# Kernel optimization log

Measured on AMD Instinct MI355X. Metric: run time of the kernel, lower is better.

The kernel has to match this reference:

```python
import jax, jax.numpy as jnp
import numpy as np

DIM = 1536
HEADS = 12
HEAD_DIM = 128
SEQ = 3120
FRAME = 1560
EPS = 1e-6


def _rmsnorm(x, gamma, eps=EPS):
    var = jnp.mean(jnp.square(x), axis=-1, keepdims=True)
    return x * jax.lax.rsqrt(var + eps) * gamma


def _rope(x, cos, sin):
    # x: [B,S,H,D], cos/sin: [S, D//2]; rotate interleaved pairs (Wan-style)
    xr = x.reshape(x.shape[:-1] + (x.shape[-1] // 2, 2))
    x1, x2 = xr[..., 0], xr[..., 1]
    c = cos[None, :, None, :]
    s = sin[None, :, None, :]
    o1 = x1 * c - x2 * s
    o2 = x1 * s + x2 * c
    return jnp.stack([o1, o2], axis=-1).reshape(x.shape)


def setup_inputs() -> dict:
    key = jax.random.key(0)
    ks = jax.random.split(key, 8)
    pos = jnp.arange(SEQ, dtype=jnp.float32)[:, None]
    inv_freq = 1.0 / (10000.0 ** (jnp.arange(0, HEAD_DIM // 2, dtype=jnp.float32) / (HEAD_DIM // 2)))
    ang = pos * inv_freq[None, :]
    return {
        "hidden_states": jax.random.normal(ks[0], (1, SEQ, DIM), jnp.float32),
        "freqs_cos": jnp.cos(ang),
        "freqs_sin": jnp.sin(ang),
        "w_qkv": jax.random.normal(ks[1], (DIM, 3 * DIM), jnp.float32) * (DIM ** -0.5),
        "b_qkv": jnp.zeros((3 * DIM,), jnp.float32),
        "g_q": jnp.ones((DIM,), jnp.float32),
        "g_k": jnp.ones((DIM,), jnp.float32),
        "w_out": jax.random.normal(ks[2], (DIM, DIM), jnp.float32) * (DIM ** -0.5),
        "b_out": jnp.zeros((DIM,), jnp.float32),
        "frame_len": FRAME,
    }


def reference(hidden_states, freqs_cos, freqs_sin, w_qkv, b_qkv, g_q, g_k, w_out, b_out, frame_len):
    B, S, _ = hidden_states.shape
    qkv = hidden_states @ w_qkv + b_qkv  # [B,S,3*DIM]
    q, k, v = jnp.split(qkv, 3, axis=-1)
    q = _rmsnorm(q, g_q)
    k = _rmsnorm(k, g_k)
    q = q.reshape(B, S, HEADS, HEAD_DIM)
    k = k.reshape(B, S, HEADS, HEAD_DIM)
    v = v.reshape(B, S, HEADS, HEAD_DIM)
    q = _rope(q, freqs_cos, freqs_sin)
    k = _rope(k, freqs_cos, freqs_sin)
    # block-wise causal mask over frames of frame_len tokens
    blk = jnp.arange(S) // frame_len
    mask = blk[None, :] <= blk[:, None]  # [Sq, Sk]
    scale = 1.0 / jnp.sqrt(jnp.float32(HEAD_DIM))
    scores = jnp.einsum("bqhd,bkhd->bhqk", q, k) * scale
    scores = jnp.where(mask[None, None], scores, jnp.float32(-1e30))
    probs = jax.nn.softmax(scores, axis=-1)
    out = jnp.einsum("bhqk,bkhd->bqhd", probs, v)
    out = out.reshape(B, S, HEADS * HEAD_DIM)
    return out @ w_out + b_out
```

## Files before the change

### kernel.cpp

```cpp
#include <hip/hip_runtime.h>
#include <hip/hip_bf16.h>
#include <stdint.h>

#define SEQ_LEN 3120
#define DIM 1536
#define QKV_N 4608
#define HEADS 12
#define HEAD_DIM 128
#define FRAME_LEN 1560
#define SM_SCALE 0.08838834764831845f
#define LOG2E 1.4426950408889634f
#define FMAXC2 43.280851226669165f
#define BQ 256

#if __has_builtin(__builtin_amdgcn_exp2f)
#define FEXP2(x) __builtin_amdgcn_exp2f(x)
#else
#define FEXP2(x) exp2f(x)
#endif

typedef short short8 __attribute__((ext_vector_type(8)));
typedef float f32x4 __attribute__((ext_vector_type(4)));
typedef float f32x16 __attribute__((ext_vector_type(16)));

__device__ __forceinline__ unsigned short f2bf(float x) {
    union { float f; unsigned u; } v; v.f = x;
    unsigned r = v.u + 0x7fffu + ((v.u >> 16) & 1u);
    return (unsigned short)(r >> 16);
}
__device__ __forceinline__ float bf2f(unsigned short b) {
    union { unsigned u; float f; } v; v.u = ((unsigned)b) << 16;
    return v.f;
}
__device__ __forceinline__ unsigned pk2bf(float a, float b) {
    __hip_bfloat162 h = __float22bfloat162_rn(make_float2(a, b));
    union { __hip_bfloat162 h2; unsigned u; } v; v.h2 = h;
    return v.u;
}

__device__ __forceinline__ void async16(void* lds, const void* g) {
    __builtin_amdgcn_global_load_lds(
        (const __attribute__((address_space(1))) unsigned int*)g,
        (__attribute__((address_space(3))) unsigned int*)lds, 16, 0, 0);
}

__device__ __forceinline__ void transpose_tile(
    const float* __restrict__ in, unsigned short* __restrict__ out,
    int R, int C, int c0, int r0, float (*T)[65], int tid)
{
    const int rl = tid >> 4, cl = (tid & 15) * 4;
#pragma unroll
    for (int i = 0; i < 4; ++i) {
        const int row = r0 + rl + i * 16;
        float4 v = *(const float4*)&in[(size_t)row * C + c0 + cl];
        T[cl + 0][rl + i * 16] = v.x; T[cl + 1][rl + i * 16] = v.y;
        T[cl + 2][rl + i * 16] = v.z; T[cl + 3][rl + i * 16] = v.w;
    }
    __syncthreads();
    const int oc = tid >> 2, ob = (tid & 3) * 16;
    union { unsigned short t[16]; uint4 u[2]; } p;
#pragma unroll
    for (int j = 0; j < 16; ++j) p.t[j] = f2bf(T[oc][ob + j]);
    uint4* dst = (uint4*)&out[(size_t)(c0 + oc) * R + r0 + ob];
    dst[0] = p.u[0];
    dst[1] = p.u[1];
}

__global__ __launch_bounds__(256) void prep_kernel(
    const float* __restrict__ hs, unsigned short* __restrict__ hsb,
    const float* __restrict__ w_qkv, unsigned short* __restrict__ wqkvT,
    const float* __restrict__ w_out, unsigned short* __restrict__ woutT)
{
    __shared__ float T[64][65];
    const int bid = blockIdx.x;
    const int tid = threadIdx.x;
    if (bid < 2340) {
        const int i = bid * 256 + tid;
        const float4 a = ((const float4*)hs)[i * 2];
        const float4 b = ((const float4*)hs)[i * 2 + 1];
        union { unsigned short t[8]; uint4 u; } p;
        p.t[0] = f2bf(a.x); p.t[1] = f2bf(a.y); p.t[2] = f2bf(a.z); p.t[3] = f2bf(a.w);
        p.t[4] = f2bf(b.x); p.t[5] = f2bf(b.y); p.t[6] = f2bf(b.z); p.t[7] = f2bf(b.w);
        ((uint4*)hsb)[i] = p.u;
    } else if (bid < 4068) {
        const int t = bid - 2340;
        transpose_tile(w_qkv, wqkvT, DIM, QKV_N, (t % 72) * 64, (t / 72) * 64, T, tid);
    } else {
        const int t = bid - 4068;
        transpose_tile(w_out, woutT, DIM, DIM, (t % 24) * 64, (t / 24) * 64, T, tid);
    }
}

__global__ __launch_bounds__(256, 2) void gemm_bt_kernel(
    const unsigned short* __restrict__ A, const unsigned short* __restrict__ Bt,
    const float* __restrict__ bias, float* __restrict__ C, int M, int N, int K,
    int ntp, int spx)
{
    __shared__ short As[2][4096];
    __shared__ short Bs[2][4096];

    const int xcd = blockIdx.x & 7;
    const int idx = (xcd & 1) * spx + (blockIdx.x >> 3);
    const int mtiles = (M + 127) >> 7;
    if (idx >= ntp * mtiles) return;
    const int m0 = (idx / ntp) * 128;
    const int n0 = ((xcd >> 1) * ntp + idx % ntp) * 128;

    const int tid = threadIdx.x;
    const int w = tid >> 6, l = tid & 63;
    const int wr = w >> 1, wc = w & 1;
    const int lhi = l >> 4, llo = l & 15;

    f32x4 acc[4][4];
#pragma unroll
    for (int i = 0; i < 4; ++i)
#pragma unroll
        for (int j = 0; j < 4; ++j) acc[i][j] = f32x4{0.f, 0.f, 0.f, 0.f};

    const int c0i = (w * 2) * 64 + l, c1i = c0i + 64;
    const unsigned short* gA0 = A + (size_t)min(m0 + (c0i >> 2), M - 1) * K + (c0i & 3) * 8;
    const unsigned short* gA1 = A + (size_t)min(m0 + (c1i >> 2), M - 1) * K + (c1i & 3) * 8;
    const unsigned short* gB0 = Bt + (size_t)(n0 + (c0i >> 2)) * K + (c0i & 3) * 8;
    const unsigned short* gB1 = Bt + (size_t)(n0 + (c1i >> 2)) * K + (c1i & 3) * 8;

    const int aoff = (wr * 64 + llo) * 32 + lhi * 8;
    const int boff = (wc * 64 + llo) * 32 + lhi * 8;

    auto stage = [&](int k0, int b) {
        async16(As[b] + (w * 2 + 0) * 512, gA0 + k0);
        async16(As[b] + (w * 2 + 1) * 512, gA1 + k0);
        async16(Bs[b] + (w * 2 + 0) * 512, gB0 + k0);
        async16(Bs[b] + (w * 2 + 1) * 512, gB1 + k0);
    };

    const int nk = K >> 5;
    stage(0, 0);
    for (int t = 0; t < nk; ++t) {
        __syncthreads();
        if (t + 1 < nk) stage((t + 1) * 32, (t + 1) & 1);
        const short* A_ = As[t & 1];
        const short* B_ = Bs[t & 1];
        short8 af[4], bf[4];
#pragma unroll
        for (int mt = 0; mt < 4; ++mt) af[mt] = *(const short8*)&A_[aoff + mt * 512];
#pragma unroll
        for (int nt = 0; nt < 4; ++nt) bf[nt] = *(const short8*)&B_[boff + nt * 512];
#pragma unroll
        for (int mt = 0; mt < 4; ++mt)
#pragma unroll
            for (int nt = 0; nt < 4; ++nt)
                acc[mt][nt] = __builtin_amdgcn_mfma_f32_16x16x32_bf16(af[mt], bf[nt], acc[mt][nt], 0, 0, 0);
    }

#pragma unroll
    for (int mt = 0; mt < 4; ++mt)
#pragma unroll
        for (int ri = 0; ri < 4; ++ri) {
            const int row = m0 + wr * 64 + mt * 16 + lhi * 4 + ri;
            if (row < M) {
#pragma unroll
                for (int nt = 0; nt < 4; ++nt) {
                    const int col = n0 + wc * 64 + nt * 16 + llo;
                    C[(size_t)row * N + col] = acc[mt][nt][ri] + bias[col];
                }
            }
        }
}

__global__ __launch_bounds__(512, 2) void gemm256_bf16_kernel(
    const unsigned short* __restrict__ A, const unsigned short* __restrict__ Bt,
    const float* __restrict__ bias, unsigned short* __restrict__ C,
    int M, int N, int K)
{
    __shared__ short LDS[65536];

    const int mtiles = (M + 255) >> 8;
    const int nwg = mtiles * (N >> 8);
    const int q = nwg >> 3, r = nwg & 7;
    const int xcd = blockIdx.x & 7;
    const int g0 = (xcd < r) ? xcd * (q + 1) : r * (q + 1) + (xcd - r) * q;
    const int g = g0 + (int)(blockIdx.x >> 3);
    const int m0 = (g % mtiles) * 256;
    const int n0 = (g / mtiles) * 256;

    const int tid = threadIdx.x;
    const int w = tid >> 6, l = tid & 63;
    const int wr = w >> 2, wc = w & 3;
    const int lhi = l >> 4, llo = l & 15;

    f32x4 acc[8][4];
#pragma unroll
    for (int i = 0; i < 8; ++i)
#pragma unroll
        for (int j = 0; j < 4; ++j) acc[i][j] = f32x4{0.f, 0.f, 0.f, 0.f};

    const unsigned short* gsrc[8];
#pragma unroll
    for (int j = 0; j < 4; ++j) {
        const int c = (j * 8 + w) * 64 + l;
        const int row = c >> 3, ks = c & 7;
        gsrc[j] = A + (size_t)min(m0 + row, M - 1) * K + (ks ^ (row & 7)) * 8;
    }
#pragma unroll
    for (int j = 0; j < 4; ++j) {
        const int c = (j * 8 + w) * 64 + l;
        const int row = c >> 3, ks = c & 7;
        gsrc[4 + j] = Bt + (size_t)min(n0 + row, N - 1) * K + (ks ^ (row & 7)) * 8;
    }

    auto stageAll = [&](int kt, int b) {
        short* dst = LDS + b * 32768;
#pragma unroll
        for (int j = 0; j < 4; ++j)
            async16(dst + (j * 8 + w) * 512, gsrc[j] + kt * 64);
#pragma unroll
        for (int j = 0; j < 4; ++j)
            async16(dst + 16384 + (j * 8 + w) * 512, gsrc[4 + j] + kt * 64);
    };

    const int nk = K >> 6;
    stageAll(0, 0);
    asm volatile("s_waitcnt vmcnt(0)\n\ts_barrier" ::: "memory");

    for (int t = 0; t < nk; ++t) {
        if (t + 1 < nk) stageAll(t + 1, (t + 1) & 1);
        const short* Ab = LDS + (t & 1) * 32768;
        const short* Bb = Ab + 16384;
#pragma unroll
        for (int ph = 0; ph < 2; ++ph) {
            short8 bfr[4];
#pragma unroll
            for (int nt = 0; nt < 4; ++nt) {
                const int rb = wc * 64 + nt * 16 + llo;
                bfr[nt] = *(const short8*)&Bb[rb * 64 + ((ph * 4 + lhi) ^ (rb & 7)) * 8];
            }
#pragma unroll
            for (int mh = 0; mh < 2; ++mh) {
                short8 afr[4];
#pragma unroll
                for (int mt = 0; mt < 4; ++mt) {
                    const int ra = wr * 128 + mh * 64 + mt * 16 + llo;
                    afr[mt] = *(const short8*)&Ab[ra * 64 + ((ph * 4 + lhi) ^ (ra & 7)) * 8];
                }
                __builtin_amdgcn_s_setprio(1);
#pragma unroll
                for (int mt = 0; mt < 4; ++mt)
#pragma unroll
                    for (int nt = 0; nt < 4; ++nt)
                        acc[mh * 4 + mt][nt] = __builtin_amdgcn_mfma_f32_16x16x32_bf16(
                            afr[mt], bfr[nt], acc[mh * 4 + mt][nt], 0, 0, 0);
                __builtin_amdgcn_s_setprio(0);
            }
        }
        asm volatile("s_waitcnt vmcnt(0)\n\ts_barrier" ::: "memory");
    }

#pragma unroll
    for (int mi = 0; mi < 8; ++mi)
#pragma unroll
        for (int ri = 0; ri < 4; ++ri) {
            const int row = m0 + wr * 128 + mi * 16 + lhi * 4 + ri;
            if (row < M) {
#pragma unroll
                for (int nt = 0; nt < 4; ++nt) {
                    const int col = n0 + wc * 64 + nt * 16 + llo;
                    C[(size_t)row * N + col] = f2bf(acc[mi][nt][ri] + bias[col]);
                }
            }
        }
}

__global__ __launch_bounds__(256) void rope_vt_kernel(
    const unsigned short* __restrict__ qkvb, const float* __restrict__ gq,
    const float* __restrict__ gk, const float* __restrict__ cosf,
    const float* __restrict__ sinf, unsigned short* __restrict__ qb,
    unsigned short* __restrict__ kb, unsigned short* __restrict__ vt)
{
    __shared__ unsigned short T[128][72];
    __shared__ float wq[4], wk[4];
    const int bid = blockIdx.x;
    const int tid = threadIdx.x;

    if (bid < SEQ_LEN) {
        const int s = bid;
        const unsigned short* qrow = qkvb + (size_t)s * QKV_N;
        const unsigned short* krow = qrow + DIM;

        float2 qp[3], kp[3];
        float ssq_q = 0.f, ssq_k = 0.f;
#pragma unroll
        for (int j = 0; j < 3; ++j) {
            const int p = tid + j * 256;
            const unsigned uq = *(const unsigned*)(qrow + 2 * p);
            const unsigned uk = *(const unsigned*)(krow + 2 * p);
            qp[j] = make_float2(bf2f((unsigned short)(uq & 0xffff)), bf2f((unsigned short)(uq >> 16)));
            kp[j] = make_float2(bf2f((unsigned short)(uk & 0xffff)), bf2f((unsigned short)(uk >> 16)));
            ssq_q += qp[j].x * qp[j].x + qp[j].y * qp[j].y;
            ssq_k += kp[j].x * kp[j].x + kp[j].y * kp[j].y;
        }
#pragma unroll
        for (int off = 32; off > 0; off >>= 1) {
            ssq_q += __shfl_down(ssq_q, off);
            ssq_k += __shfl_down(ssq_k, off);
        }
        const int wave = tid >> 6, lane = tid & 63;
        if (lane == 0) { wq[wave] = ssq_q; wk[wave] = ssq_k; }
        __syncthreads();
        const float tq = wq[0] + wq[1] + wq[2] + wq[3];
        const float tk = wk[0] + wk[1] + wk[2] + wk[3];
        const float inv_q = rsqrtf(tq * (1.0f / DIM) + 1e-6f) * (SM_SCALE * LOG2E);
        const float inv_k = rsqrtf(tk * (1.0f / DIM) + 1e-6f);

#pragma unroll
        for (int j = 0; j < 3; ++j) {
            const int p = tid + j * 256;
            const int fi = p & 63;
            const float c = cosf[s * 64 + fi];
            const float si = sinf[s * 64 + fi];
            {
                const float y1 = qp[j].x * inv_q * gq[2 * p];
                const float y2 = qp[j].y * inv_q * gq[2 * p + 1];
                *(unsigned*)&qb[(size_t)s * DIM + 2 * p] = pk2bf(y1 * c - y2 * si, y1 * si + y2 * c);
            }
            {
                const float y1 = kp[j].x * inv_k * gk[2 * p];
                const float y2 = kp[j].y * inv_k * gk[2 * p + 1];
                *(unsigned*)&kb[(size_t)s * DIM + 2 * p] = pk2bf(y1 * c - y2 * si, y1 * si + y2 * c);
            }
        }
    } else {
        const int t = bid - SEQ_LEN;
        const int s0 = (t % 49) * 64;
        const int h = t / 49;
        const int rl = tid >> 2, cb = (tid & 3) * 32;
        const int row = min(s0 + rl, SEQ_LEN - 1);
#pragma unroll
        for (int i = 0; i < 4; ++i) {
            const int d = cb + i * 8;
            union { uint4 u; unsigned short t8[8]; } v;
            v.u = *(const uint4*)&qkvb[(size_t)row * QKV_N + 2 * DIM + h * HEAD_DIM + d];
#pragma unroll
            for (int j = 0; j < 8; ++j) T[d + j][rl] = v.t8[j];
        }
        __syncthreads();
        const int od = tid >> 1, ob = (tid & 1) * 32;
        const size_t orow = (size_t)(h * HEAD_DIM + od) * SEQ_LEN;
#pragma unroll
        for (int v8 = 0; v8 < 4; ++v8) {
            const int s = s0 + ob + v8 * 8;
            if (s < SEQ_LEN) {
                union { unsigned short t8[8]; uint4 u; } pk;
#pragma unroll
                for (int j = 0; j < 8; ++j) pk.t8[j] = T[od][ob + v8 * 8 + j];
                *(uint4*)&vt[orow + s] = pk.u;
            }
        }
    }
}

__global__ __launch_bounds__(512, 2) void attn_part_kernel(
    const unsigned short* __restrict__ qb, const unsigned short* __restrict__ kb,
    const unsigned short* __restrict__ vt, unsigned short* __restrict__ part_o,
    float* __restrict__ part_ml, unsigned short* __restrict__ attb)
{
    __shared__ short KV[40960];

    const int bid = blockIdx.x;
    const int xcd = bid & 7;
    const int slot = bid >> 3;
    int h, bx;
    if (slot < 20) { h = xcd; bx = slot; }
    else { h = 8 + (xcd >> 1); bx = (xcd & 1) * 10 + (slot - 20); }

    const int tid = threadIdx.x;
    const int w = tid >> 6;
    const int l = tid & 63;
    int tile, split, nsp;
    if (bx < 6) { tile = bx; split = 0; nsp = 1; }
    else { const int b2 = bx - 6; tile = 6 + (b2 >> 1); split = b2 & 1; nsp = 2; }
    const int q0 = tile * BQ;
    const int lhi = l >> 5;
    const int llo = l & 31;

#pragma unroll
    for (int s = 0; s < 8; ++s) {
        const int c = (s * 8 + w) * 64 + l;
        const int row = c >> 4, g = c & 15;
        const int gr = min(q0 + row, SEQ_LEN - 1);
        async16(KV + (s * 8 + w) * 512, qb + (size_t)gr * DIM + h * HEAD_DIM + g * 8);
    }
    __syncthreads();
    short8 qf[8];
#pragma unroll
    for (int ds = 0; ds < 8; ++ds)
        qf[ds] = *(const short8*)&KV[(w * 32 + llo) * 128 + ds * 16 + lhi * 8];
    __syncthreads();

    const int myq = q0 + w * 32 + llo;
    const int mylimit = (myq < FRAME_LEN) ? FRAME_LEN : SEQ_LEN;
    const int wave_lim = (q0 + w * 32 < FRAME_LEN) ? FRAME_LEN : SEQ_LEN;
    const int Lmax = (tile < 6) ? FRAME_LEN : SEQ_LEN;
    const int nch = (Lmax + 63) >> 6;
    const int kc0 = ((split * nch) / nsp) * 64;
    const int kc1 = (((split + 1) * nch) / nsp) * 64;
    const int nchunks = (kc1 - kc0) >> 6;

    float l_run = 0.f;
    f32x16 o[4];
#pragma unroll
    for (int mt = 0; mt < 4; ++mt)
#pragma unroll
        for (int r = 0; r < 16; ++r) o[mt][r] = 0.f;

    int krloc[2], kcol[2], vcol[2], lof[2];
    size_t vrow[2];
#pragma unroll
    for (int s = 0; s < 2; ++s) {
        const int c = (s * 8 + w) * 64 + l;
        const int kr = c >> 4;
        krloc[s] = kr;
        kcol[s] = h * HEAD_DIM + (((c & 15) ^ (kr & 7)) * 8);
        const int d = c >> 3;
        vrow[s] = (size_t)(h * HEAD_DIM + d) * SEQ_LEN;
        vcol[s] = ((c & 7) ^ (d & 7)) * 8;
        lof[s] = (s * 8 + w) * 512;
    }

    auto issueK = [&](int kc, int b) {
#pragma unroll
        for (int s = 0; s < 2; ++s) {
            const int gr = min(kc + krloc[s], SEQ_LEN - 1);
            async16(KV + b * 8192 + lof[s], kb + (size_t)gr * DIM + kcol[s]);
        }
    };
    auto issueV = [&](int kc, int t) {
#pragma unroll
        for (int s = 0; s < 2; ++s) {
            const int col = min(kc + vcol[s], SEQ_LEN - 8);
            async16(KV + 16384 + t * 8192 + lof[s], vt + vrow[s] + col);
        }
    };

    auto qkt = [&](f32x16* st, int b) {
        const short* Kb = KV + b * 8192;
#pragma unroll
        for (int r = 0; r < 16; ++r) { st[0][r] = 0.f; st[1][r] = 0.f; }
        __builtin_amdgcn_s_setprio(1);
#pragma unroll
        for (int ds = 0; ds < 8; ++ds) {
            const int gd = ds * 2 + lhi;
#pragma unroll
            for (int kt = 0; kt < 2; ++kt) {
                const int krow = kt * 32 + llo;
                short8 kf = *(const short8*)&Kb[krow * 128 + ((gd ^ (krow & 7)) * 8)];
                st[kt] = __builtin_amdgcn_mfma_f32_32x32x16_bf16(kf, qf[ds], st[kt], 0, 0, 0);
            }
        }
        __builtin_amdgcn_s_setprio(0);
    };

    auto sm_pv = [&](f32x16* st, int kc, int t) {
        if (kc + 64 > wave_lim) {
#pragma unroll
            for (int kt = 0; kt < 2; ++kt)
#pragma unroll
                for (int r = 0; r < 16; ++r) {
                    const int kg = kc + kt * 32 + (r & 3) + 8 * (r >> 2) + 4 * lhi;
                    if (kg >= mylimit) st[kt][r] = -3.0e38f;
                }
        }
        float rs = 0.f;
        unsigned p16[2][8];
#pragma unroll
        for (int kt = 0; kt < 2; ++kt)
#pragma unroll
            for (int r2 = 0; r2 < 8; ++r2) {
                const float p0 = FEXP2(st[kt][2 * r2] - FMAXC2);
                const float p1 = FEXP2(st[kt][2 * r2 + 1] - FMAXC2);
                rs += p0 + p1;
                p16[kt][r2] = pk2bf(p0, p1);
            }
        l_run += rs;

        const short* Vb = KV + 16384 + t * 8192;
#pragma unroll
        for (int kblk = 0; kblk < 4; ++kblk) {
            const int tt = kblk >> 1;
            const int i0 = (kblk & 1) * 4;
            union { unsigned u[4]; short8 s8; } pf;
#if __has_builtin(__builtin_amdgcn_permlane32_swap)
            {
                auto s02 = __builtin_amdgcn_permlane32_swap(
                    p16[tt][i0 + 0], p16[tt][i0 + 2], false, false);
                auto s13 = __builtin_amdgcn_permlane32_swap(
                    p16[tt][i0 + 1], p16[tt][i0 + 3], false, false);
                pf.u[0] = s02[0]; pf.u[1] = s13[0];
                pf.u[2] = s02[1]; pf.u[3] = s13[1];
            }
#else
            {
                const int dk    = ((kblk & 1) * 2 + lhi) * 2;
                const int dsend = ((kblk & 1) * 2 + (1 - lhi)) * 2;
                const unsigned r0 = __shfl_xor(p16[tt][dsend], 32);
                const unsigned r1 = __shfl_xor(p16[tt][dsend + 1], 32);
                if (lhi == 0) { pf.u[0] = p16[tt][dk]; pf.u[1] = p16[tt][dk + 1]; pf.u[2] = r0; pf.u[3] = r1; }
                else          { pf.u[0] = r0; pf.u[1] = r1; pf.u[2] = p16[tt][dk]; pf.u[3] = p16[tt][dk + 1]; }
            }
#endif
            __builtin_amdgcn_s_setprio(1);
#pragma unroll
            for (int mt = 0; mt < 4; ++mt) {
                const int vd = mt * 32 + llo;
                short8 vf = *(const short8*)&Vb[vd * 64 + (((kblk * 2 + lhi) ^ (vd & 7)) * 8)];
                o[mt] = __builtin_amdgcn_mfma_f32_32x32x16_bf16(vf, pf.s8, o[mt], 0, 0, 0);
            }
            __builtin_amdgcn_s_setprio(0);
        }
    };

    issueK(kc0, 0); issueV(kc0, 0);
    if (nchunks > 1) { issueK(kc0 + 64, 1); issueV(kc0 + 64, 1); }
    __syncthreads();
    f32x16 stC[2];
    qkt(stC, 0);

    int vcur = 0;
    for (int i = 0, kc = kc0; i < nchunks; ++i, kc += 64) {
        __syncthreads();
        if (i + 2 < nchunks) {
            issueK(kc + 128, i & 1);
            int vt2 = vcur + 2; if (vt2 >= 3) vt2 -= 3;
            issueV(kc + 128, vt2);
        }
        f32x16 stN[2];
        if (i + 1 < nchunks) qkt(stN, (i + 1) & 1);
        sm_pv(stC, kc, vcur);
        if (i + 1 < nchunks) { stC[0] = stN[0]; stC[1] = stN[1]; }
        vcur = (vcur == 2) ? 0 : vcur + 1;
    }

    const float l_tot = l_run + __shfl_xor(l_run, 32);
    const int qloc = w * 32 + llo;
    const float inv = (l_tot > 0.f) ? 1.0f / l_tot : 0.f;
    if (nsp == 1) {
        unsigned short* op = attb + (size_t)(q0 + qloc) * DIM + h * HEAD_DIM + 4 * lhi;
#pragma unroll
        for (int mt = 0; mt < 4; ++mt)
#pragma unroll
            for (int g = 0; g < 4; ++g) {
                uint2 u;
                u.x = pk2bf(o[mt][4 * g + 0] * inv, o[mt][4 * g + 1] * inv);
                u.y = pk2bf(o[mt][4 * g + 2] * inv, o[mt][4 * g + 3] * inv);
                *(uint2*)&op[mt * 32 + 8 * g] = u;
            }
    } else {
        const int slot_o = bx * HEADS + h;
        unsigned short* op = part_o + (size_t)slot_o * (BQ * HEAD_DIM) + qloc * HEAD_DIM + 4 * lhi;
#pragma unroll
        for (int mt = 0; mt < 4; ++mt)
#pragma unroll
            for (int g = 0; g < 4; ++g) {
                uint2 u;
                u.x = pk2bf(o[mt][4 * g + 0] * inv, o[mt][4 * g + 1] * inv);
                u.y = pk2bf(o[mt][4 * g + 2] * inv, o[mt][4 * g + 3] * inv);
                *(uint2*)&op[mt * 32 + 8 * g] = u;
            }
        if (lhi == 0) part_ml[(size_t)slot_o * BQ + qloc] = l_tot;
    }
}

__global__ __launch_bounds__(256) void attn_combine_kernel(
    const unsigned short* __restrict__ part_o, const float* __restrict__ part_ml,
    unsigned short* __restrict__ attb)
{
    const int h = blockIdx.y;
    const int q = 1536 + blockIdx.x * 8 + (threadIdx.x >> 5);
    const int dq = (threadIdx.x & 31) * 4;
    const int tile = q >> 8, qloc = q & 255;
    const int base_bx = 6 + (tile - 6) * 2;

    float W = 0.f;
    float acc[4] = {0.f, 0.f, 0.f, 0.f};
#pragma unroll
    for (int s = 0; s < 2; ++s) {
        const int slot = (base_bx + s) * HEADS + h;
        const float w = part_ml[(size_t)slot * BQ + qloc];
        if (w > 0.f) {
            W += w;
            const unsigned short* po = part_o +
                (size_t)slot * (BQ * HEAD_DIM) + qloc * HEAD_DIM + dq;
            uint2 u = *(const uint2*)po;
            acc[0] += w * bf2f((unsigned short)(u.x & 0xffff));
            acc[1] += w * bf2f((unsigned short)(u.x >> 16));
            acc[2] += w * bf2f((unsigned short)(u.y & 0xffff));
            acc[3] += w * bf2f((unsigned short)(u.y >> 16));
        }
    }
    const float inv = 1.0f / W;
    uint2 pk;
    pk.x = pk2bf(acc[0] * inv, acc[1] * inv);
    pk.y = pk2bf(acc[2] * inv, acc[3] * inv);
    *(uint2*)&attb[(size_t)q * DIM + h * HEAD_DIM + dq] = pk;
}

extern "C" void kernel_launch(void* const* d_in, const int* in_sizes, int n_in,
                              void* d_out, int out_size, void* d_ws, size_t ws_size,
                              hipStream_t stream)
{
    const float* hs    = (const float*)d_in[0];
    const float* cosf  = (const float*)d_in[1];
    const float* sinf  = (const float*)d_in[2];
    const float* w_qkv = (const float*)d_in[3];
    const float* b_qkv = (const float*)d_in[4];
    const float* g_q   = (const float*)d_in[5];
    const float* g_k   = (const float*)d_in[6];
    const float* w_out = (const float*)d_in[7];
    const float* b_out = (const float*)d_in[8];

    char* base = (char*)d_ws;
    unsigned short* qb     = (unsigned short*)base;
    unsigned short* kb     = (unsigned short*)(base + 9584640);
    unsigned short* vt     = (unsigned short*)(base + 19169280);
    unsigned short* hsb    = vt;
    unsigned short* qkvb   = (unsigned short*)(base + 28753920);
    unsigned short* part_o = (unsigned short*)(base + 28753920);
    float*          part_ml= (float*)(base + 60211200);
    unsigned short* wqkvT  = (unsigned short*)(base + 81469440);
    unsigned short* attb   = wqkvT;
    unsigned short* woutT  = (unsigned short*)(base + 95625216);
    float* outp = (float*)d_out;

    prep_kernel<<<4644, 256, 0, stream>>>(hs, hsb, w_qkv, wqkvT, w_out, woutT);
    gemm256_bf16_kernel<<<234, 512, 0, stream>>>(
        hsb, wqkvT, b_qkv, qkvb, SEQ_LEN, QKV_N, DIM);
    rope_vt_kernel<<<SEQ_LEN + 49 * HEADS, 256, 0, stream>>>(
        qkvb, g_q, g_k, cosf, sinf, qb, kb, vt);
    attn_part_kernel<<<240, 512, 0, stream>>>(qb, kb, vt, part_o, part_ml, attb);
    attn_combine_kernel<<<dim3((SEQ_LEN - 1536) / 8, HEADS), 256, 0, stream>>>(
        part_o, part_ml, attb);
    gemm_bt_kernel<<<304, 256, 0, stream>>>(
        attb, woutT, b_out, outp, SEQ_LEN, DIM, DIM, 3, 38);
}
```

Before: 280.1 us.

## Reorder attention loop: softmax first, then fused QK^T and PV MFMA burst

```diff
diff --git a/kernel.cpp b/kernel.cpp
--- a/kernel.cpp
+++ b/kernel.cpp
@@ -387,13 +387,15 @@
         const int c = (s * 8 + w) * 64 + l;
         const int row = c >> 4, g = c & 15;
         const int gr = min(q0 + row, SEQ_LEN - 1);
-        async16(KV + (s * 8 + w) * 512, qb + (size_t)gr * DIM + h * HEAD_DIM + g * 8);
+        async16(KV + (s * 8 + w) * 512,
+                qb + (size_t)gr * DIM + h * HEAD_DIM + (g ^ (row & 7)) * 8);
     }
     __syncthreads();
     short8 qf[8];
 #pragma unroll
     for (int ds = 0; ds < 8; ++ds)
-        qf[ds] = *(const short8*)&KV[(w * 32 + llo) * 128 + ds * 16 + lhi * 8];
+        qf[ds] = *(const short8*)&KV[(w * 32 + llo) * 128 +
+                                     (((ds * 2 + lhi) ^ (llo & 7)) * 8)];
     __syncthreads();
 
     const int myq = q0 + w * 32 + llo;
@@ -445,7 +447,6 @@
         const short* Kb = KV + b * 8192;
 #pragma unroll
         for (int r = 0; r < 16; ++r) { st[0][r] = 0.f; st[1][r] = 0.f; }
-        __builtin_amdgcn_s_setprio(1);
 #pragma unroll
         for (int ds = 0; ds < 8; ++ds) {
             const int gd = ds * 2 + lhi;
@@ -456,10 +457,9 @@
                 st[kt] = __builtin_amdgcn_mfma_f32_32x32x16_bf16(kf, qf[ds], st[kt], 0, 0, 0);
             }
         }
-        __builtin_amdgcn_s_setprio(0);
     };
 
-    auto sm_pv = [&](f32x16* st, int kc, int t) {
+    auto sm = [&](f32x16* st, int kc, short8* pfout) {
         if (kc + 64 > wave_lim) {
 #pragma unroll
             for (int kt = 0; kt < 2; ++kt)
@@ -469,7 +469,7 @@
                     if (kg >= mylimit) st[kt][r] = -3.0e38f;
                 }
         }
-        float rs = 0.f;
+        float rsA = 0.f, rsB = 0.f;
         unsigned p16[2][8];
 #pragma unroll
         for (int kt = 0; kt < 2; ++kt)
@@ -477,12 +477,11 @@
             for (int r2 = 0; r2 < 8; ++r2) {
                 const float p0 = FEXP2(st[kt][2 * r2] - FMAXC2);
                 const float p1 = FEXP2(st[kt][2 * r2 + 1] - FMAXC2);
-                rs += p0 + p1;
+                if (kt == 0) rsA += p0 + p1; else rsB += p0 + p1;
                 p16[kt][r2] = pk2bf(p0, p1);
             }
-        l_run += rs;
-
-        const short* Vb = KV + 16384 + t * 8192;
+        l_run += rsA + rsB;
+
 #pragma unroll
         for (int kblk = 0; kblk < 4; ++kblk) {
             const int tt = kblk >> 1;
@@ -507,14 +506,20 @@
                 else          { pf.u[0] = r0; pf.u[1] = r1; pf.u[2] = p16[tt][dk]; pf.u[3] = p16[tt][dk + 1]; }
             }
 #endif
-            __builtin_amdgcn_s_setprio(1);
+            pfout[kblk] = pf.s8;
+        }
+    };
+
+    auto pv = [&](const short8* pf, int t) {
+        const short* Vb = KV + 16384 + t * 8192;
+#pragma unroll
+        for (int kblk = 0; kblk < 4; ++kblk) {
 #pragma unroll
             for (int mt = 0; mt < 4; ++mt) {
                 const int vd = mt * 32 + llo;
                 short8 vf = *(const short8*)&Vb[vd * 64 + (((kblk * 2 + lhi) ^ (vd & 7)) * 8)];
-                o[mt] = __builtin_amdgcn_mfma_f32_32x32x16_bf16(vf, pf.s8, o[mt], 0, 0, 0);
-            }
-            __builtin_amdgcn_s_setprio(0);
+                o[mt] = __builtin_amdgcn_mfma_f32_32x32x16_bf16(vf, pf[kblk], o[mt], 0, 0, 0);
+            }
         }
     };
 
@@ -532,10 +537,20 @@
             int vt2 = vcur + 2; if (vt2 >= 3) vt2 -= 3;
             issueV(kc + 128, vt2);
         }
-        f32x16 stN[2];
-        if (i + 1 < nchunks) qkt(stN, (i + 1) & 1);
-        sm_pv(stC, kc, vcur);
-        if (i + 1 < nchunks) { stC[0] = stN[0]; stC[1] = stN[1]; }
+        short8 pf[4];
+        sm(stC, kc, pf);
+        if (i + 1 < nchunks) {
+            f32x16 stN[2];
+            __builtin_amdgcn_s_setprio(1);
+            qkt(stN, (i + 1) & 1);
+            pv(pf, vcur);
+            __builtin_amdgcn_s_setprio(0);
+            stC[0] = stN[0]; stC[1] = stN[1];
+        } else {
+            __builtin_amdgcn_s_setprio(1);
+            pv(pf, vcur);
+            __builtin_amdgcn_s_setprio(0);
+        }
         vcur = (vcur == 2) ? 0 : vcur + 1;
     }
 
```

New measurement: 319.3 us. 1.14x slower.

## Rework output GEMM with 64-wide K tiles, swizzled LDS, and contiguous XCD tile mapping

Applied to the files above, without the earlier changes.

```diff
diff --git a/kernel.cpp b/kernel.cpp
--- a/kernel.cpp
+++ b/kernel.cpp
@@ -91,20 +91,23 @@
     }
 }
 
-__global__ __launch_bounds__(256, 2) void gemm_bt_kernel(
+__global__ __launch_bounds__(256, 2) void gemm128_f32_kernel(
     const unsigned short* __restrict__ A, const unsigned short* __restrict__ Bt,
-    const float* __restrict__ bias, float* __restrict__ C, int M, int N, int K,
-    int ntp, int spx)
-{
-    __shared__ short As[2][4096];
-    __shared__ short Bs[2][4096];
-
+    const float* __restrict__ bias, float* __restrict__ C, int M, int N, int K)
+{
+    __shared__ short LDS[32768];
+
+    const int mtiles = (M + 127) >> 7;
+    const int nwg = mtiles * (N >> 7);
+    const int q = nwg >> 3, r = nwg & 7;
     const int xcd = blockIdx.x & 7;
-    const int idx = (xcd & 1) * spx + (blockIdx.x >> 3);
-    const int mtiles = (M + 127) >> 7;
-    if (idx >= ntp * mtiles) return;
-    const int m0 = (idx / ntp) * 128;
-    const int n0 = ((xcd >> 1) * ntp + idx % ntp) * 128;
+    const int cnt = q + (xcd < r ? 1 : 0);
+    const int li = blockIdx.x >> 3;
+    if (li >= cnt) return;
+    const int g0 = (xcd < r) ? xcd * (q + 1) : r * (q + 1) + (xcd - r) * q;
+    const int g = g0 + li;
+    const int m0 = (g % mtiles) * 128;
+    const int n0 = (g / mtiles) * 128;
 
     const int tid = threadIdx.x;
     const int w = tid >> 6, l = tid & 63;
@@ -117,39 +120,61 @@
 #pragma unroll
         for (int j = 0; j < 4; ++j) acc[i][j] = f32x4{0.f, 0.f, 0.f, 0.f};
 
-    const int c0i = (w * 2) * 64 + l, c1i = c0i + 64;
-    const unsigned short* gA0 = A + (size_t)min(m0 + (c0i >> 2), M - 1) * K + (c0i & 3) * 8;
-    const unsigned short* gA1 = A + (size_t)min(m0 + (c1i >> 2), M - 1) * K + (c1i & 3) * 8;
-    const unsigned short* gB0 = Bt + (size_t)(n0 + (c0i >> 2)) * K + (c0i & 3) * 8;
-    const unsigned short* gB1 = Bt + (size_t)(n0 + (c1i >> 2)) * K + (c1i & 3) * 8;
-
-    const int aoff = (wr * 64 + llo) * 32 + lhi * 8;
-    const int boff = (wc * 64 + llo) * 32 + lhi * 8;
-
-    auto stage = [&](int k0, int b) {
-        async16(As[b] + (w * 2 + 0) * 512, gA0 + k0);
-        async16(As[b] + (w * 2 + 1) * 512, gA1 + k0);
-        async16(Bs[b] + (w * 2 + 0) * 512, gB0 + k0);
-        async16(Bs[b] + (w * 2 + 1) * 512, gB1 + k0);
+    const unsigned short* gsrc[8];
+#pragma unroll
+    for (int j = 0; j < 4; ++j) {
+        const int c = (j * 4 + w) * 64 + l;
+        const int row = c >> 3, ks = c & 7;
+        gsrc[j] = A + (size_t)min(m0 + row, M - 1) * K + (ks ^ (row & 7)) * 8;
+    }
+#pragma unroll
+    for (int j = 0; j < 4; ++j) {
+        const int c = (j * 4 + w) * 64 + l;
+        const int row = c >> 3, ks = c & 7;
+        gsrc[4 + j] = Bt + (size_t)min(n0 + row, N - 1) * K + (ks ^ (row & 7)) * 8;
+    }
+
+    auto stageAll = [&](int kt, int b) {
+        short* dst = LDS + b * 16384;
+#pragma unroll
+        for (int j = 0; j < 4; ++j)
+            async16(dst + (j * 4 + w) * 512, gsrc[j] + kt * 64);
+#pragma unroll
+        for (int j = 0; j < 4; ++j)
+            async16(dst + 8192 + (j * 4 + w) * 512, gsrc[4 + j] + kt * 64);
     };
 
-    const int nk = K >> 5;
-    stage(0, 0);
+    const int nk = K >> 6;
+    stageAll(0, 0);
+    asm volatile("s_waitcnt vmcnt(0)\n\ts_barrier" ::: "memory");
+
     for (int t = 0; t < nk; ++t) {
-        __syncthreads();
-        if (t + 1 < nk) stage((t + 1) * 32, (t + 1) & 1);
-        const short* A_ = As[t & 1];
-        const short* B_ = Bs[t & 1];
-        short8 af[4], bf[4];
-#pragma unroll
-        for (int mt = 0; mt < 4; ++mt) af[mt] = *(const short8*)&A_[aoff + mt * 512];
-#pragma unroll
-        for (int nt = 0; nt < 4; ++nt) bf[nt] = *(const short8*)&B_[boff + nt * 512];
-#pragma unroll
-        for (int mt = 0; mt < 4; ++mt)
-#pragma unroll
-            for (int nt = 0; nt < 4; ++nt)
-                acc[mt][nt] = __builtin_amdgcn_mfma_f32_16x16x32_bf16(af[mt], bf[nt], acc[mt][nt], 0, 0, 0);
+        if (t + 1 < nk) stageAll(t + 1, (t + 1) & 1);
+        const short* Ab = LDS + (t & 1) * 16384;
+        const short* Bb = Ab + 8192;
+#pragma unroll
+        for (int ph = 0; ph < 2; ++ph) {
+            short8 bfr[4], afr[4];
+#pragma unroll
+            for (int nt = 0; nt < 4; ++nt) {
+                const int rb = wc * 64 + nt * 16 + llo;
+                bfr[nt] = *(const short8*)&Bb[rb * 64 + ((ph * 4 + lhi) ^ (rb & 7)) * 8];
+            }
+#pragma unroll
+            for (int mt = 0; mt < 4; ++mt) {
+                const int ra = wr * 64 + mt * 16 + llo;
+                afr[mt] = *(const short8*)&Ab[ra * 64 + ((ph * 4 + lhi) ^ (ra & 7)) * 8];
+            }
+            __builtin_amdgcn_s_setprio(1);
+#pragma unroll
+            for (int mt = 0; mt < 4; ++mt)
+#pragma unroll
+                for (int nt = 0; nt < 4; ++nt)
+                    acc[mt][nt] = __builtin_amdgcn_mfma_f32_16x16x32_bf16(
+                        afr[mt], bfr[nt], acc[mt][nt], 0, 0, 0);
+            __builtin_amdgcn_s_setprio(0);
+        }
+        asm volatile("s_waitcnt vmcnt(0)\n\ts_barrier" ::: "memory");
     }
 
 #pragma unroll
@@ -387,13 +412,15 @@
         const int c = (s * 8 + w) * 64 + l;
         const int row = c >> 4, g = c & 15;
         const int gr = min(q0 + row, SEQ_LEN - 1);
-        async16(KV + (s * 8 + w) * 512, qb + (size_t)gr * DIM + h * HEAD_DIM + g * 8);
+        async16(KV + (s * 8 + w) * 512,
+                qb + (size_t)gr * DIM + h * HEAD_DIM + (g ^ (row & 7)) * 8);
     }
     __syncthreads();
     short8 qf[8];
 #pragma unroll
     for (int ds = 0; ds < 8; ++ds)
-        qf[ds] = *(const short8*)&KV[(w * 32 + llo) * 128 + ds * 16 + lhi * 8];
+        qf[ds] = *(const short8*)&KV[(w * 32 + llo) * 128 +
+                                     (((ds * 2 + lhi) ^ (llo & 7)) * 8)];
     __syncthreads();
 
     const int myq = q0 + w * 32 + llo;
@@ -469,7 +496,7 @@
                     if (kg >= mylimit) st[kt][r] = -3.0e38f;
                 }
         }
-        float rs = 0.f;
+        float rsA = 0.f, rsB = 0.f;
         unsigned p16[2][8];
 #pragma unroll
         for (int kt = 0; kt < 2; ++kt)
@@ -477,10 +504,10 @@
             for (int r2 = 0; r2 < 8; ++r2) {
                 const float p0 = FEXP2(st[kt][2 * r2] - FMAXC2);
                 const float p1 = FEXP2(st[kt][2 * r2 + 1] - FMAXC2);
-                rs += p0 + p1;
+                if (kt == 0) rsA += p0 + p1; else rsB += p0 + p1;
                 p16[kt][r2] = pk2bf(p0, p1);
             }
-        l_run += rs;
+        l_run += rsA + rsB;
 
         const short* Vb = KV + 16384 + t * 8192;
 #pragma unroll
@@ -638,6 +665,6 @@
     attn_part_kernel<<<240, 512, 0, stream>>>(qb, kb, vt, part_o, part_ml, attb);
     attn_combine_kernel<<<dim3((SEQ_LEN - 1536) / 8, HEADS), 256, 0, stream>>>(
         part_o, part_ml, attb);
-    gemm_bt_kernel<<<304, 256, 0, stream>>>(
-        attb, woutT, b_out, outp, SEQ_LEN, DIM, DIM, 3, 38);
-}
+    gemm128_f32_kernel<<<304, 256, 0, stream>>>(
+        attb, woutT, b_out, outp, SEQ_LEN, DIM, DIM);
+}
```

Result: faster. 268.4 us, median of 4 (-4.2%).
